# Kernel optimization log

Measured on AMD Instinct MI355X. Metric: run time of the kernel, lower is better.

The kernel has to match this reference:

```python
import jax, jax.numpy as jnp
import numpy as np

B, T, C = 2, 2048, 1024
H = 16
D = C // H  # head_dim = 64


def setup_inputs() -> dict:
    key = jax.random.key(0)
    ks = jax.random.split(key, 9)
    s = 0.02
    return {
        "x": jax.random.normal(ks[0], (B, T, C), dtype=jnp.float32),
        "Wq": jax.random.normal(ks[1], (C, C), dtype=jnp.float32) * s,
        "bq": jax.random.normal(ks[2], (C,), dtype=jnp.float32) * s,
        "Wk": jax.random.normal(ks[3], (C, C), dtype=jnp.float32) * s,
        "bk": jax.random.normal(ks[4], (C,), dtype=jnp.float32) * s,
        "Wv": jax.random.normal(ks[5], (C, C), dtype=jnp.float32) * s,
        "bv": jax.random.normal(ks[6], (C,), dtype=jnp.float32) * s,
        "Wo": jax.random.normal(ks[7], (C, C), dtype=jnp.float32) * s,
        "bo": jax.random.normal(ks[8], (C,), dtype=jnp.float32) * s,
    }


def reference(x, Wq, bq, Wk, bk, Wv, bv, Wo, bo):
    b, t, c = x.shape
    h, d = H, c // H
    # torch nn.Linear: y = x @ W.T + b
    q = (x @ Wq.T + bq).reshape(b, t, h, d).transpose(0, 2, 1, 3)  # [B,H,T,D]
    k = (x @ Wk.T + bk).reshape(b, t, h, d).transpose(0, 2, 1, 3)
    v = (x @ Wv.T + bv).reshape(b, t, h, d).transpose(0, 2, 1, 3)

    scores = jnp.einsum("bhqd,bhkd->bhqk", q, k) / jnp.sqrt(jnp.float32(d))
    causal = jnp.tril(jnp.ones((t, t), dtype=bool))  # [T,T]
    scores = jnp.where(causal[None, None, :, :], scores, -jnp.inf)
    attn = jax.nn.softmax(scores, axis=-1)  # [B,H,T,T]

    out = jnp.einsum("bhqk,bhkd->bhqd", attn, v)  # [B,H,T,D]
    out = out.transpose(0, 2, 1, 3).reshape(b, t, c)
    out = out @ Wo.T + bo
    return out
```

## Files before the change

kernel.cpp:

```cpp
#include <hip/hip_runtime.h>
#include <hip/hip_bf16.h>

using u16 = unsigned short;
using u32 = unsigned int;
using short8  = __attribute__((ext_vector_type(8))) short;
using short4v = __attribute__((ext_vector_type(4))) short;
using floatx4 = __attribute__((ext_vector_type(4))) float;

#define TT 2048
#define CC 1024
#define HH 16
#define DD 64
#define BBATCH 2
#define MM (BBATCH*TT)

#define QSCALE 0.18033688011112042f

__device__ __forceinline__ u16 f2bf(float f) {
    u32 u = __float_as_uint(f);
    u += 0x7fffu + ((u >> 16) & 1u);
    return (u16)(u >> 16);
}
__device__ __forceinline__ void gll16(const u16* g, u16* l) {
    __builtin_amdgcn_global_load_lds((const __attribute__((address_space(1))) void*)g,
                                     (__attribute__((address_space(3))) void*)l, 16, 0, 0);
}

__global__ __launch_bounds__(256) void cast_all(const float* __restrict__ x,
    const float* __restrict__ Wq, const float* __restrict__ Wk,
    const float* __restrict__ Wv, const float* __restrict__ Wo,
    u16* __restrict__ xb, u16* __restrict__ wqb, u16* __restrict__ wkb,
    u16* __restrict__ wvb, u16* __restrict__ wob)
{
    int i = blockIdx.x * 256 + threadIdx.x;
    const float* src; u16* dst; int off;
    if (i < 1048576) { src = x; dst = xb; off = i; }
    else {
        int j = i - 1048576;
        int s = j >> 18;
        off = j & 262143;
        src = (s == 0) ? Wq : (s == 1) ? Wk : (s == 2) ? Wv : Wo;
        dst = (s == 0) ? wqb : (s == 1) ? wkb : (s == 2) ? wvb : wob;
    }
    float4 v = ((const float4*)src)[off];
    u16 r[4];
    r[0] = f2bf(v.x); r[1] = f2bf(v.y); r[2] = f2bf(v.z); r[3] = f2bf(v.w);
    ((ushort4*)dst)[off] = *(ushort4*)r;
}

__global__ __launch_bounds__(256, 3) void qkv_gemm(const u16* __restrict__ xb,
    const u16* __restrict__ wq, const u16* __restrict__ wk, const u16* __restrict__ wv,
    const float* __restrict__ bq, const float* __restrict__ bk, const float* __restrict__ bv,
    u16* __restrict__ q, u16* __restrict__ k, u16* __restrict__ vt)
{
    __shared__ u16 As[128*32];
    __shared__ u16 Bs[128*32];
    const int K = CC;
    int z = blockIdx.z;
    const u16* W = (z == 0) ? wq : (z == 1) ? wk : wv;
    const float* bias = (z == 0) ? bq : (z == 1) ? bk : bv;
    float outscale = (z == 0) ? QSCALE : 1.0f;

    int tid = threadIdx.x;
    int m0 = blockIdx.y * 128;
    int n0 = blockIdx.x * 128;
    int lane = tid & 63;
    int w  = tid >> 6;
    int wm = (w >> 1) * 64;
    int wn = (w & 1) * 64;
    int lm = lane & 15;
    int lq = lane >> 4;

    floatx4 acc[4][4];
#pragma unroll
    for (int i = 0; i < 4; ++i)
#pragma unroll
        for (int j = 0; j < 4; ++j)
            acc[i][j] = (floatx4){0.f, 0.f, 0.f, 0.f};

    const u16* ag = xb + (size_t)(m0 + (tid >> 2)) * K + (tid & 3) * 8;
    const u16* wg = W  + (size_t)(n0 + (tid >> 2)) * K + (tid & 3) * 8;
    u16* asl = As + tid * 8;
    u16* bsl = Bs + tid * 8;

    for (int k0 = 0; k0 < K; k0 += 32) {
        __syncthreads();
        gll16(ag + k0,           asl);
        gll16(ag + 64*K + k0,    asl + 2048);
        gll16(wg + k0,           bsl);
        gll16(wg + 64*K + k0,    bsl + 2048);
        __syncthreads();
        short8 af[4], bfr[4];
#pragma unroll
        for (int t = 0; t < 4; ++t) {
            af[t]  = *(const short8*)(As + (wm + t*16 + lm)*32 + lq*8);
            bfr[t] = *(const short8*)(Bs + (wn + t*16 + lm)*32 + lq*8);
        }
#pragma unroll
        for (int i = 0; i < 4; ++i)
#pragma unroll
            for (int j = 0; j < 4; ++j)
                acc[i][j] = __builtin_amdgcn_mfma_f32_16x16x32_bf16(af[i], bfr[j], acc[i][j], 0, 0, 0);
    }

    if (z < 2) {
        u16* outp = (z == 0) ? q : k;
#pragma unroll
        for (int j = 0; j < 4; ++j) {
            int col = n0 + wn + j*16 + lm;
            float bv2 = bias[col];
            int h_ = col >> 6, d_ = col & 63;
#pragma unroll
            for (int i = 0; i < 4; ++i) {
#pragma unroll
                for (int r = 0; r < 4; ++r) {
                    int row = m0 + wm + i*16 + lq*4 + r;
                    float val = (acc[i][j][r] + bv2) * outscale;
                    int b_ = row >> 11, t_ = row & (TT-1);
                    outp[(((size_t)(b_*HH + h_) * TT + t_) * DD) + d_] = f2bf(val);
                }
            }
        }
    } else {
#pragma unroll
        for (int j = 0; j < 4; ++j) {
            int col = n0 + wn + j*16 + lm;
            float bv2 = bias[col];
            int h_ = col >> 6, d_ = col & 63;
#pragma unroll
            for (int i = 0; i < 4; ++i) {
                int row0 = m0 + wm + i*16 + lq*4;
                int b_ = row0 >> 11, t_ = row0 & (TT-1);
                u16 rr[4];
#pragma unroll
                for (int r = 0; r < 4; ++r) rr[r] = f2bf(acc[i][j][r] + bv2);
                *(ushort4*)(vt + ((size_t)(b_*HH + h_) * DD + d_) * TT + t_) = *(ushort4*)rr;
            }
        }
    }
}

__global__ __launch_bounds__(256, 4) void o_gemm(const u16* __restrict__ A, const u16* __restrict__ W,
                                                 const float* __restrict__ bias, float* __restrict__ outp)
{
    __shared__ u16 As[128*32];
    __shared__ u16 Bs[64*32];
    const int K = CC;
    int tid = threadIdx.x;
    int m0 = blockIdx.y * 128;
    int n0 = blockIdx.x * 64;
    int lane = tid & 63;
    int w  = tid >> 6;
    int lm = lane & 15;
    int lq = lane >> 4;

    floatx4 acc[2][4];
#pragma unroll
    for (int i = 0; i < 2; ++i)
#pragma unroll
        for (int j = 0; j < 4; ++j)
            acc[i][j] = (floatx4){0.f, 0.f, 0.f, 0.f};

    const u16* ag = A + (size_t)(m0 + (tid >> 2)) * K + (tid & 3) * 8;
    const u16* wg = W + (size_t)(n0 + (tid >> 2)) * K + (tid & 3) * 8;
    u16* asl = As + tid * 8;
    u16* bsl = Bs + tid * 8;

    for (int k0 = 0; k0 < K; k0 += 32) {
        __syncthreads();
        gll16(ag + k0,        asl);
        gll16(ag + 64*K + k0, asl + 2048);
        gll16(wg + k0,        bsl);
        __syncthreads();
        short8 af[2], bfr[4];
#pragma unroll
        for (int i = 0; i < 2; ++i)
            af[i] = *(const short8*)(As + (w*32 + i*16 + lm)*32 + lq*8);
#pragma unroll
        for (int j = 0; j < 4; ++j)
            bfr[j] = *(const short8*)(Bs + (j*16 + lm)*32 + lq*8);
#pragma unroll
        for (int i = 0; i < 2; ++i)
#pragma unroll
            for (int j = 0; j < 4; ++j)
                acc[i][j] = __builtin_amdgcn_mfma_f32_16x16x32_bf16(af[i], bfr[j], acc[i][j], 0, 0, 0);
    }

#pragma unroll
    for (int j = 0; j < 4; ++j) {
        int col = n0 + j*16 + lm;
        float bv2 = bias[col];
#pragma unroll
        for (int i = 0; i < 2; ++i) {
#pragma unroll
            for (int r = 0; r < 4; ++r) {
                int row = m0 + w*32 + i*16 + lq*4 + r;
                outp[(size_t)row * CC + col] = acc[i][j][r] + bv2;
            }
        }
    }
}

__global__ __launch_bounds__(256, 3) void attn_mfma(const u16* __restrict__ qg, const u16* __restrict__ kg,
                                                    const u16* __restrict__ vtg, u16* __restrict__ attnb)
{
    __shared__ u16 Kf[2][8*64*8];
    __shared__ u16 Vf[2][8*64*8];

    int tid = threadIdx.x;
    int lane = tid & 63;
    int w = tid >> 6;
    int lm = lane & 15;
    int lq = lane >> 4;
    int x = blockIdx.x;
    int qt = (x < 8) ? x : (23 - x);
    int bh = blockIdx.y;
    int b_ = bh >> 4, h_ = bh & 15;
    int q0 = qt * 128;

    const size_t basek  = (size_t)bh * TT * DD;
    const size_t basevt = (size_t)bh * DD * TT;

    short8 aq[2][2];
    {
        const u16* qbase = qg + basek + (size_t)(q0 + w*32 + lm) * DD + lq*8;
#pragma unroll
        for (int i = 0; i < 2; ++i)
#pragma unroll
            for (int ks = 0; ks < 2; ++ks)
                aq[i][ks] = *(const short8*)(qbase + i*16*DD + ks*32);
    }

    floatx4 oacc[2][4];
    floatx4 lacc[2];
#pragma unroll
    for (int i = 0; i < 2; ++i) {
        lacc[i] = (floatx4){0.f, 0.f, 0.f, 0.f};
#pragma unroll
        for (int j = 0; j < 4; ++j)
            oacc[i][j] = (floatx4){0.f, 0.f, 0.f, 0.f};
    }
    short4v ones;
#pragma unroll
    for (int j = 0; j < 4; ++j) ones[j] = (short)0x3F80;

    const u16* kgl = kg + basek + (size_t)(w*16 + lm) * DD + lq*8;
    u16* kd0a = &Kf[0][(w*2+0)*512] + lane*8;
    u16* kd1a = &Kf[0][(w*2+1)*512] + lane*8;
    u16* kd0b = &Kf[1][(w*2+0)*512] + lane*8;
    u16* kd1b = &Kf[1][(w*2+1)*512] + lane*8;

    int vr = tid >> 2;
    int kbv = tid & 3;
    const u16* vsrc = vtg + basevt + (size_t)vr * TT + kbv*16;
    int jd2v = vr >> 5, jdparv = (vr >> 4) & 1, lmv = vr & 15;
    u32 vbase = ((u32)(kbv*2 + jd2v)*64 + lmv) * 8 + jdparv*4;

    int nkt = 2*qt + 2;
    int wrowmax = q0 + w*32 + 31;

    gll16(kgl,      kd0a);
    gll16(kgl + 32, kd1a);
    uint4 va = *(const uint4*)(vsrc);
    uint4 vb = *(const uint4*)(vsrc + 8);

    for (int kt = 0; kt < nkt; ++kt) {
        int p = kt & 1;
        {
            u16* vd = &Vf[p][0] + vbase;
            *(uint2*)(vd)           = make_uint2(va.x, va.y);
            *(uint2*)(vd + 16*8)    = make_uint2(va.z, va.w);
            *(uint2*)(vd + 32*8)    = make_uint2(vb.x, vb.y);
            *(uint2*)(vd + 48*8)    = make_uint2(vb.z, vb.w);
        }
        __syncthreads();

        if (kt + 1 < nkt) {
            const u16* kn = kgl + (size_t)(kt+1)*64*DD;
            if (p == 0) { gll16(kn, kd0b); gll16(kn + 32, kd1b); }
            else        { gll16(kn, kd0a); gll16(kn + 32, kd1a); }
            va = *(const uint4*)(vsrc + (kt+1)*64);
            vb = *(const uint4*)(vsrc + (kt+1)*64 + 8);
        }

        int kbase = kt * 64;
        if (kbase <= wrowmax) {
            short8 kf[4][2];
#pragma unroll
            for (int jn = 0; jn < 4; ++jn)
#pragma unroll
                for (int ks = 0; ks < 2; ++ks)
                    kf[jn][ks] = *(const short8*)(&Kf[p][(jn*2+ks)*512] + lane*8);

            floatx4 st[2][4];
#pragma unroll
            for (int i = 0; i < 2; ++i)
#pragma unroll
                for (int jn = 0; jn < 4; ++jn)
                    st[i][jn] = (floatx4){0.f, 0.f, 0.f, 0.f};
#pragma unroll
            for (int jn = 0; jn < 4; ++jn)
#pragma unroll
                for (int i = 0; i < 2; ++i) {
                    st[i][jn] = __builtin_amdgcn_mfma_f32_16x16x32_bf16(kf[jn][0], aq[i][0], st[i][jn], 0, 0, 0);
                    st[i][jn] = __builtin_amdgcn_mfma_f32_16x16x32_bf16(kf[jn][1], aq[i][1], st[i][jn], 0, 0, 0);
                }

            short4v ap[2][4];
#pragma unroll
            for (int i = 0; i < 2; ++i) {
                int qrow = q0 + w*32 + i*16 + lm;
                if (kbase + 63 > q0 + w*32 + i*16) {
#pragma unroll
                    for (int jn = 0; jn < 4; ++jn)
#pragma unroll
                        for (int r = 0; r < 4; ++r) {
                            int key = kbase + jn*16 + lq*4 + r;
                            if (key > qrow) st[i][jn][r] = -__builtin_inff();
                        }
                }
#pragma unroll
                for (int jn = 0; jn < 4; ++jn) {
#pragma unroll
                    for (int r = 0; r < 4; ++r)
                        st[i][jn][r] = __builtin_amdgcn_exp2f(st[i][jn][r]);
                    u32 lo = __builtin_amdgcn_perm(__float_as_uint(st[i][jn][1]),
                                                   __float_as_uint(st[i][jn][0]), 0x07060302u);
                    u32 hi = __builtin_amdgcn_perm(__float_as_uint(st[i][jn][3]),
                                                   __float_as_uint(st[i][jn][2]), 0x07060302u);
                    uint2 pk = make_uint2(lo, hi);
                    ap[i][jn] = __builtin_bit_cast(short4v, pk);
                }
            }

#pragma unroll
            for (int kb = 0; kb < 4; ++kb) {
#pragma unroll
                for (int jd2 = 0; jd2 < 2; ++jd2) {
                    short8 vv = *(const short8*)(&Vf[p][(kb*2+jd2)*512] + lane*8);
                    short4v vlo, vhi;
#pragma unroll
                    for (int j = 0; j < 4; ++j) { vlo[j] = vv[j]; vhi[j] = vv[j+4]; }
#pragma unroll
                    for (int i = 0; i < 2; ++i) {
                        oacc[i][jd2*2]   = __builtin_amdgcn_mfma_f32_16x16x16bf16_1k(ap[i][kb], vlo, oacc[i][jd2*2],   0, 0, 0);
                        oacc[i][jd2*2+1] = __builtin_amdgcn_mfma_f32_16x16x16bf16_1k(ap[i][kb], vhi, oacc[i][jd2*2+1], 0, 0, 0);
                    }
                }
#pragma unroll
                for (int i = 0; i < 2; ++i)
                    lacc[i] = __builtin_amdgcn_mfma_f32_16x16x16bf16_1k(ap[i][kb], ones, lacc[i], 0, 0, 0);
            }
        }
    }

#pragma unroll
    for (int i = 0; i < 2; ++i) {
#pragma unroll
        for (int r = 0; r < 4; ++r) {
            float il = 1.f / lacc[i][r];
            int qrow = q0 + w*32 + i*16 + lq*4 + r;
            u16* orow = attnb + ((size_t)(b_*TT + qrow)) * CC + h_*DD + lm;
#pragma unroll
            for (int jd = 0; jd < 4; ++jd)
                orow[jd*16] = f2bf(oacc[i][jd][r] * il);
        }
    }
}

extern "C" void kernel_launch(void* const* d_in, const int* in_sizes, int n_in,
                              void* d_out, int out_size, void* d_ws, size_t ws_size,
                              hipStream_t stream)
{
    const float* x  = (const float*)d_in[0];
    const float* Wq = (const float*)d_in[1];
    const float* bq = (const float*)d_in[2];
    const float* Wk = (const float*)d_in[3];
    const float* bk = (const float*)d_in[4];
    const float* Wv = (const float*)d_in[5];
    const float* bv = (const float*)d_in[6];
    const float* Wo = (const float*)d_in[7];
    const float* bo = (const float*)d_in[8];
    float* out = (float*)d_out;

    char* ws = (char*)d_ws;
    u16* xb   = (u16*)(ws);
    u16* wqb  = (u16*)(ws + (size_t)( 8<<20));
    u16* wkb  = (u16*)(ws + (size_t)(10<<20));
    u16* wvb  = (u16*)(ws + (size_t)(12<<20));
    u16* wob  = (u16*)(ws + (size_t)(14<<20));
    u16* q    = (u16*)(ws + (size_t)(16<<20));
    u16* k    = (u16*)(ws + (size_t)(24<<20));
    u16* vt   = (u16*)(ws + (size_t)(32<<20));
    u16* attnb = xb;

    cast_all<<<dim3(8192), dim3(256), 0, stream>>>(x, Wq, Wk, Wv, Wo, xb, wqb, wkb, wvb, wob);

    dim3 gq(CC/128, MM/128, 3);
    qkv_gemm<<<gq, dim3(256), 0, stream>>>(xb, wqb, wkb, wvb, bq, bk, bv, q, k, vt);

    attn_mfma<<<dim3(16, BBATCH*HH), dim3(256), 0, stream>>>(q, k, vt, attnb);

    dim3 go(CC/64, MM/128);
    o_gemm<<<go, dim3(256), 0, stream>>>(attnb, wob, bo, out);
}
```

Measured before the change: 191.1 us.

## Split causal attention KV range across blocks and store V in fragment layout

Attention work is split along the KV dimension (split-K style) using a slot table that assigns up to four parts per query tile, giving a 40x32 grid with more balanced per-block work. A new finalize kernel sums the partial outputs and row sums, then normalizes. The QKV GEMM now writes V directly in MFMA fragment order, so the attention kernel loads V straight into registers and no longer stages it through LDS. This cuts shared memory use and allows higher occupancy. The cost is an extra kernel launch, extra global traffic for the bf16 partials, and some rounding error because partials are stored in bf16 before they are summed. Skipping the running max is only safe because the softmax has no max subtraction, the same as before.

Result: slower. 268.1 us (+40.3%).

```diff
diff --git a/kernel.cpp b/kernel.cpp
--- a/kernel.cpp
+++ b/kernel.cpp
@@ -21,10 +21,24 @@
     u += 0x7fffu + ((u >> 16) & 1u);
     return (u16)(u >> 16);
 }
+__device__ __forceinline__ float bf2f(u16 s) {
+    return __uint_as_float(((u32)s) << 16);
+}
 __device__ __forceinline__ void gll16(const u16* g, u16* l) {
     __builtin_amdgcn_global_load_lds((const __attribute__((address_space(1))) void*)g,
                                      (__attribute__((address_space(3))) void*)l, 16, 0, 0);
 }
+
+__constant__ unsigned char SLOT_TBL[40] = {
+    12, 28, 29, 42,  0,
+    44, 45, 46,  8,  4,
+    57, 59, 24, 20, 16,
+    60, 25, 37, 38, 17,
+    40, 41, 49, 51, 21,
+    52, 53, 54, 55, 33,
+    61, 62, 34, 36, 50,
+    63, 56, 58, 32, 48,
+};
 
 __global__ __launch_bounds__(256) void cast_all(const float* __restrict__ x,
     const float* __restrict__ Wq, const float* __restrict__ Wk,
@@ -51,7 +65,7 @@
 __global__ __launch_bounds__(256, 3) void qkv_gemm(const u16* __restrict__ xb,
     const u16* __restrict__ wq, const u16* __restrict__ wk, const u16* __restrict__ wv,
     const float* __restrict__ bq, const float* __restrict__ bk, const float* __restrict__ bv,
-    u16* __restrict__ q, u16* __restrict__ k, u16* __restrict__ vt)
+    u16* __restrict__ q, u16* __restrict__ k, u16* __restrict__ vfm)
 {
     __shared__ u16 As[128*32];
     __shared__ u16 Bs[128*32];
@@ -127,14 +141,21 @@
             int col = n0 + wn + j*16 + lm;
             float bv2 = bias[col];
             int h_ = col >> 6, d_ = col & 63;
+            int ch_hi = (d_ >> 5) ;
+            int hi4   = ((d_ >> 4) & 1) * 4;
+            int lmv   = d_ & 15;
 #pragma unroll
             for (int i = 0; i < 4; ++i) {
                 int row0 = m0 + wm + i*16 + lq*4;
-                int b_ = row0 >> 11, t_ = row0 & (TT-1);
+                int b_ = row0 >> 11, tl = row0 & (TT-1);
+                int kt = tl >> 6, kb = (tl >> 4) & 3, lqv = (tl >> 2) & 3;
+                int ch = kb*2 + ch_hi;
+                int lanev = lqv*16 + lmv;
                 u16 rr[4];
 #pragma unroll
                 for (int r = 0; r < 4; ++r) rr[r] = f2bf(acc[i][j][r] + bv2);
-                *(ushort4*)(vt + ((size_t)(b_*HH + h_) * DD + d_) * TT + t_) = *(ushort4*)rr;
+                *(ushort4*)(vfm + ((size_t)(b_*HH + h_) * TT * DD)
+                                 + (((size_t)kt*8 + ch)*64 + lanev)*8 + hi4) = *(ushort4*)rr;
             }
         }
     }
@@ -201,11 +222,11 @@
     }
 }
 
-__global__ __launch_bounds__(256, 3) void attn_mfma(const u16* __restrict__ qg, const u16* __restrict__ kg,
-                                                    const u16* __restrict__ vtg, u16* __restrict__ attnb)
+__global__ __launch_bounds__(256, 4) void attn_mfma(const u16* __restrict__ qg, const u16* __restrict__ kg,
+                                                    const u16* __restrict__ vfm,
+                                                    u16* __restrict__ Opart, float* __restrict__ lpart)
 {
     __shared__ u16 Kf[2][8*64*8];
-    __shared__ u16 Vf[2][8*64*8];
 
     int tid = threadIdx.x;
     int lane = tid & 63;
@@ -213,13 +234,15 @@
     int lm = lane & 15;
     int lq = lane >> 4;
     int x = blockIdx.x;
-    int qt = (x < 8) ? x : (23 - x);
+    int e = SLOT_TBL[(x & 7)*5 + (x >> 3)];
+    int qt = e >> 2, part = e & 3;
+    int P = (qt >> 2) + 1;
+    int nkt = 2*qt + 2;
+    int kt0 = (part*nkt)/P, kt1 = ((part+1)*nkt)/P;
     int bh = blockIdx.y;
-    int b_ = bh >> 4, h_ = bh & 15;
     int q0 = qt * 128;
 
-    const size_t basek  = (size_t)bh * TT * DD;
-    const size_t basevt = (size_t)bh * DD * TT;
+    const size_t basek = (size_t)bh * TT * DD;
 
     short8 aq[2][2];
     {
@@ -245,46 +268,33 @@
     for (int j = 0; j < 4; ++j) ones[j] = (short)0x3F80;
 
     const u16* kgl = kg + basek + (size_t)(w*16 + lm) * DD + lq*8;
-    u16* kd0a = &Kf[0][(w*2+0)*512] + lane*8;
-    u16* kd1a = &Kf[0][(w*2+1)*512] + lane*8;
-    u16* kd0b = &Kf[1][(w*2+0)*512] + lane*8;
-    u16* kd1b = &Kf[1][(w*2+1)*512] + lane*8;
-
-    int vr = tid >> 2;
-    int kbv = tid & 3;
-    const u16* vsrc = vtg + basevt + (size_t)vr * TT + kbv*16;
-    int jd2v = vr >> 5, jdparv = (vr >> 4) & 1, lmv = vr & 15;
-    u32 vbase = ((u32)(kbv*2 + jd2v)*64 + lmv) * 8 + jdparv*4;
-
-    int nkt = 2*qt + 2;
     int wrowmax = q0 + w*32 + 31;
 
-    gll16(kgl,      kd0a);
-    gll16(kgl + 32, kd1a);
-    uint4 va = *(const uint4*)(vsrc);
-    uint4 vb = *(const uint4*)(vsrc + 8);
-
-    for (int kt = 0; kt < nkt; ++kt) {
-        int p = kt & 1;
-        {
-            u16* vd = &Vf[p][0] + vbase;
-            *(uint2*)(vd)           = make_uint2(va.x, va.y);
-            *(uint2*)(vd + 16*8)    = make_uint2(va.z, va.w);
-            *(uint2*)(vd + 32*8)    = make_uint2(vb.x, vb.y);
-            *(uint2*)(vd + 48*8)    = make_uint2(vb.z, vb.w);
-        }
+    {
+        const u16* kn = kgl + (size_t)kt0*64*DD;
+        gll16(kn,      &Kf[0][(w*2+0)*512] + lane*8);
+        gll16(kn + 32, &Kf[0][(w*2+1)*512] + lane*8);
+    }
+
+    for (int kt = kt0; kt < kt1; ++kt) {
+        int p = (kt - kt0) & 1;
         __syncthreads();
-
-        if (kt + 1 < nkt) {
+        if (kt + 1 < kt1) {
             const u16* kn = kgl + (size_t)(kt+1)*64*DD;
-            if (p == 0) { gll16(kn, kd0b); gll16(kn + 32, kd1b); }
-            else        { gll16(kn, kd0a); gll16(kn + 32, kd1a); }
-            va = *(const uint4*)(vsrc + (kt+1)*64);
-            vb = *(const uint4*)(vsrc + (kt+1)*64 + 8);
+            gll16(kn,      &Kf[1-p][(w*2+0)*512] + lane*8);
+            gll16(kn + 32, &Kf[1-p][(w*2+1)*512] + lane*8);
         }
 
         int kbase = kt * 64;
         if (kbase <= wrowmax) {
+            short8 vchunk[8];
+            {
+                const u16* vb = vfm + basek + ((size_t)kt*8*64 + lane)*8;
+#pragma unroll
+                for (int ch = 0; ch < 8; ++ch)
+                    vchunk[ch] = *(const short8*)(vb + ch*512);
+            }
+
             short8 kf[4][2];
 #pragma unroll
             for (int jn = 0; jn < 4; ++jn)
@@ -337,7 +347,7 @@
             for (int kb = 0; kb < 4; ++kb) {
 #pragma unroll
                 for (int jd2 = 0; jd2 < 2; ++jd2) {
-                    short8 vv = *(const short8*)(&Vf[p][(kb*2+jd2)*512] + lane*8);
+                    short8 vv = vchunk[kb*2 + jd2];
                     short4v vlo, vhi;
 #pragma unroll
                     for (int j = 0; j < 4; ++j) { vlo[j] = vv[j]; vhi[j] = vv[j+4]; }
@@ -354,17 +364,50 @@
         }
     }
 
+    size_t slot = (size_t)(bh*16 + qt)*4 + part;
+    u16* obase = Opart + slot * (128*64);
 #pragma unroll
     for (int i = 0; i < 2; ++i) {
 #pragma unroll
         for (int r = 0; r < 4; ++r) {
-            float il = 1.f / lacc[i][r];
-            int qrow = q0 + w*32 + i*16 + lq*4 + r;
-            u16* orow = attnb + ((size_t)(b_*TT + qrow)) * CC + h_*DD + lm;
+            int row = w*32 + i*16 + lq*4 + r;
 #pragma unroll
             for (int jd = 0; jd < 4; ++jd)
-                orow[jd*16] = f2bf(oacc[i][jd][r] * il);
-        }
+                obase[row*64 + jd*16 + lm] = f2bf(oacc[i][jd][r]);
+            if (lm == 0)
+                lpart[slot*128 + row] = lacc[i][r];
+        }
+    }
+}
+
+__global__ __launch_bounds__(256) void attn_finalize(const u16* __restrict__ Opart,
+    const float* __restrict__ lpart, u16* __restrict__ attnb)
+{
+    int qt = blockIdx.x, bh = blockIdx.y;
+    int b_ = bh >> 4, h_ = bh & 15;
+    int P = (qt >> 2) + 1;
+    int tid = threadIdx.x;
+    __shared__ float lt[128];
+    size_t slot0 = (size_t)(bh*16 + qt)*4;
+    if (tid < 128) {
+        float s = 0.f;
+        for (int p2 = 0; p2 < P; ++p2) s += lpart[(slot0 + p2)*128 + tid];
+        lt[tid] = 1.f / s;
+    }
+    __syncthreads();
+#pragma unroll
+    for (int jj = 0; jj < 8; ++jj) {
+        int e4 = tid + jj*256;
+        int ei = e4 * 4;
+        int row = ei >> 6, d = ei & 63;
+        float a0 = 0.f, a1 = 0.f, a2 = 0.f, a3 = 0.f;
+        for (int p2 = 0; p2 < P; ++p2) {
+            ushort4 v = *(const ushort4*)(Opart + (slot0 + p2)*8192 + ei);
+            a0 += bf2f(v.x); a1 += bf2f(v.y); a2 += bf2f(v.z); a3 += bf2f(v.w);
+        }
+        float il = lt[row];
+        u16 rr[4] = {f2bf(a0*il), f2bf(a1*il), f2bf(a2*il), f2bf(a3*il)};
+        *(ushort4*)(attnb + ((size_t)(b_*TT + qt*128 + row))*CC + h_*DD + d) = *(ushort4*)rr;
     }
 }
 
@@ -384,22 +427,26 @@
     float* out = (float*)d_out;
 
     char* ws = (char*)d_ws;
-    u16* xb   = (u16*)(ws);
-    u16* wqb  = (u16*)(ws + (size_t)( 8<<20));
-    u16* wkb  = (u16*)(ws + (size_t)(10<<20));
-    u16* wvb  = (u16*)(ws + (size_t)(12<<20));
-    u16* wob  = (u16*)(ws + (size_t)(14<<20));
-    u16* q    = (u16*)(ws + (size_t)(16<<20));
-    u16* k    = (u16*)(ws + (size_t)(24<<20));
-    u16* vt   = (u16*)(ws + (size_t)(32<<20));
-    u16* attnb = xb;
+    u16*   xb    = (u16*)(ws);
+    u16*   wqb   = (u16*)(ws + (size_t)( 8<<20));
+    u16*   wkb   = (u16*)(ws + (size_t)(10<<20));
+    u16*   wvb   = (u16*)(ws + (size_t)(12<<20));
+    u16*   wob   = (u16*)(ws + (size_t)(14<<20));
+    u16*   q     = (u16*)(ws + (size_t)(16<<20));
+    u16*   k     = (u16*)(ws + (size_t)(24<<20));
+    u16*   vfm   = (u16*)(ws + (size_t)(32<<20));
+    u16*   Opart = (u16*)(ws + (size_t)(40<<20));
+    float* lpart = (float*)(ws + (size_t)(72<<20));
+    u16*   attnb = xb;
 
     cast_all<<<dim3(8192), dim3(256), 0, stream>>>(x, Wq, Wk, Wv, Wo, xb, wqb, wkb, wvb, wob);
 
     dim3 gq(CC/128, MM/128, 3);
-    qkv_gemm<<<gq, dim3(256), 0, stream>>>(xb, wqb, wkb, wvb, bq, bk, bv, q, k, vt);
-
-    attn_mfma<<<dim3(16, BBATCH*HH), dim3(256), 0, stream>>>(q, k, vt, attnb);
+    qkv_gemm<<<gq, dim3(256), 0, stream>>>(xb, wqb, wkb, wvb, bq, bk, bv, q, k, vfm);
+
+    attn_mfma<<<dim3(40, BBATCH*HH), dim3(256), 0, stream>>>(q, k, vfm, Opart, lpart);
+
+    attn_finalize<<<dim3(16, BBATCH*HH), dim3(256), 0, stream>>>(Opart, lpart, attnb);
 
     dim3 go(CC/64, MM/128);
     o_gemm<<<go, dim3(256), 0, stream>>>(attnb, wob, bo, out);
```
